# Kernel tuning notes

Hardware: AMD Instinct MI355X
Metric: run time of the kernel (lower is better)

## Reference

```python
import jax, jax.numpy as jnp
import numpy as np
import math

B, S, D, H, KVH = 4, 2048, 4096, 32, 8
HD = D // H          # 128
N_REP = H // KVH     # 4
MAX_S = 2048


def setup_inputs() -> dict:
    key = jax.random.key(0)
    ks = jax.random.split(key, 6)
    x = jax.random.normal(ks[0], (B, S, D), dtype=jnp.float32)
    sc = 0.02
    wq = jax.random.normal(ks[1], (D, H * HD), dtype=jnp.float32) * sc
    wk = jax.random.normal(ks[2], (D, KVH * HD), dtype=jnp.float32) * sc
    wv = jax.random.normal(ks[3], (D, KVH * HD), dtype=jnp.float32) * sc
    wo = jax.random.normal(ks[4], (H * HD, D), dtype=jnp.float32) * sc
    # RoPE tables (matches llama precompute_freqs_cis, theta=10000)
    inv_freq = 1.0 / (10000.0 ** (np.arange(0, HD, 2, dtype=np.float32) / HD))  # [HD/2]
    t = np.arange(S, dtype=np.float32)
    freqs = np.outer(t, inv_freq)  # [S, HD/2]
    cos = jnp.asarray(np.cos(freqs), dtype=jnp.float32)
    sin = jnp.asarray(np.sin(freqs), dtype=jnp.float32)
    cache_k = jnp.zeros((B, MAX_S, KVH, HD), dtype=jnp.float32)
    cache_v = jnp.zeros((B, MAX_S, KVH, HD), dtype=jnp.float32)
    return {"x": x, "wq": wq, "wk": wk, "wv": wv, "wo": wo,
            "cos": cos, "sin": sin, "cache_k": cache_k, "cache_v": cache_v,
            "start_pos": 0}


def _apply_rope(x, cos, sin):
    # x: [B, S, h, HD]; interleaved complex rotation, as torch view_as_complex
    xr = x.reshape(*x.shape[:-1], HD // 2, 2)
    x0, x1 = xr[..., 0], xr[..., 1]
    c = cos[None, :, None, :]
    s = sin[None, :, None, :]
    o0 = x0 * c - x1 * s
    o1 = x0 * s + x1 * c
    return jnp.stack([o0, o1], axis=-1).reshape(x.shape)


def reference(x, wq, wk, wv, wo, cos, sin, cache_k, cache_v, start_pos):
    bsz, seqlen, _ = x.shape
    xq = (x @ wq).reshape(bsz, seqlen, H, HD)
    xk = (x @ wk).reshape(bsz, seqlen, KVH, HD)
    xv = (x @ wv).reshape(bsz, seqlen, KVH, HD)
    xq = _apply_rope(xq, cos, sin)
    xk = _apply_rope(xk, cos, sin)
    # KV cache update then slice [:start_pos+seqlen]
    cache_k = jax.lax.dynamic_update_slice(cache_k, xk, (0, start_pos, 0, 0))
    cache_v = jax.lax.dynamic_update_slice(cache_v, xv, (0, start_pos, 0, 0))
    kv_len = start_pos + seqlen
    keys = cache_k[:, :kv_len]    # [B, K, KVH, HD]
    values = cache_v[:, :kv_len]
    # repeat_kv: expand kv heads by n_rep (GQA)
    keys = jnp.repeat(keys, N_REP, axis=2)      # [B, K, H, HD]
    values = jnp.repeat(values, N_REP, axis=2)
    scores = jnp.einsum('bqhd,bkhd->bhqk', xq, keys) / math.sqrt(HD)
    probs = jax.nn.softmax(scores.astype(jnp.float32), axis=-1).astype(xq.dtype)
    out = jnp.einsum('bhqk,bkhd->bqhd', probs, values)
    out = out.reshape(bsz, seqlen, H * HD)
    return out @ wo
```

## Files before the change

kernel.cpp:

```cpp
#include <hip/hip_runtime.h>
#include <math.h>
#include <stdint.h>

typedef unsigned short u16;
typedef __attribute__((ext_vector_type(8))) short short8;
typedef __attribute__((ext_vector_type(4))) float f32x4;

#define B_   4
#define S_   2048
#define D_   4096
#define H_   32
#define KVH_ 8
#define HD_  128
#define NQKV 6144
#define MTOT 8192
#define ATT_SCALE 0.08838834764831845f
#define DEFER_THR 90.5f

__device__ __forceinline__ float bf2f(u16 u) {
  unsigned x = ((unsigned)u) << 16;
  return __builtin_bit_cast(float, x);
}
__device__ __forceinline__ u16 f2bf(float f) {
  unsigned x = __builtin_bit_cast(unsigned, f);
  x += 0x7fffu + ((x >> 16) & 1u);
  return (u16)(x >> 16);
}
__device__ __forceinline__ unsigned pack2bf(float a, float b) {
  return (unsigned)f2bf(a) | ((unsigned)f2bf(b) << 16);
}

typedef const __attribute__((address_space(1))) void* gas1p;
typedef __attribute__((address_space(3))) void* las3p;
__device__ __forceinline__ void gload16(const void* g, void* l) {
  __builtin_amdgcn_global_load_lds((gas1p)g, (las3p)l, 16, 0, 0);
}

__device__ __forceinline__ int swz64(int row, int kc) {
  return row * 64 + ((kc ^ (row & 7)) << 3);
}
__device__ __forceinline__ int swz128(int row, int kc) {
  return row * 128 + ((kc ^ (row & 7)) << 3);
}

__global__ void cast_f32_to_bf16(const float* __restrict__ in, u16* __restrict__ out, long n) {
  long i = ((long)blockIdx.x * 256 + threadIdx.x) * 4;
  if (i >= n) return;
  float4 v = *(const float4*)(in + i);
  ushort4 o;
  o.x = f2bf(v.x); o.y = f2bf(v.y); o.z = f2bf(v.z); o.w = f2bf(v.w);
  *(ushort4*)(out + i) = o;
}

__global__ void transpose_cast(const float* __restrict__ in, u16* __restrict__ out, int K, int N) {
  __shared__ u16 tile[32][33];
  int n0 = blockIdx.x * 32, k0 = blockIdx.y * 32;
  int tx = threadIdx.x, ty = threadIdx.y;
  for (int i = ty; i < 32; i += 8)
    tile[i][tx] = f2bf(in[(long)(k0 + i) * N + n0 + tx]);
  __syncthreads();
  for (int i = ty; i < 32; i += 8)
    out[(long)(n0 + i) * K + k0 + tx] = tile[tx][i];
}

template <int OUTF32>
__global__ __launch_bounds__(512, 2) void gemm256(const u16* __restrict__ A,
                                                  const u16* __restrict__ BT,
                                                  void* __restrict__ Cout,
                                                  int M, int N, int K) {
  __shared__ u16 Ls[2][2][2][128 * 64];
  int tid = threadIdx.x, lane = tid & 63, wid = tid >> 6;
  int wm = wid >> 2, wn = wid & 3;
  int m0 = blockIdx.y * 256, n0 = blockIdx.x * 256;
  int frow = lane & 15, fk = lane >> 4;

  f32x4 acc[8][4];
#pragma unroll
  for (int i = 0; i < 8; i++)
#pragma unroll
    for (int j = 0; j < 4; j++) acc[i][j] = (f32x4){0.f, 0.f, 0.f, 0.f};

  int srow = lane >> 3;
  int sc = ((lane & 7) ^ srow) * 8;
  const u16* a0 = A + (long)(m0 + (2 * wid + 0) * 8 + srow) * K + sc;
  const u16* a1 = A + (long)(m0 + (2 * wid + 1) * 8 + srow) * K + sc;
  const u16* b0 = BT + (long)(n0 + (2 * wid + 0) * 8 + srow) * K + sc;
  const u16* b1 = BT + (long)(n0 + (2 * wid + 1) * 8 + srow) * K + sc;
  long hstep = (long)128 * K;

#define STAGE_A(buf, half, t) do {                                              \
    gload16(a0 + (half) * hstep + (long)(t) * 64, &Ls[buf][0][half][(2 * wid + 0) * 512]); \
    gload16(a1 + (half) * hstep + (long)(t) * 64, &Ls[buf][0][half][(2 * wid + 1) * 512]); \
  } while (0)
#define STAGE_B(buf, half, t) do {                                              \
    gload16(b0 + (half) * hstep + (long)(t) * 64, &Ls[buf][1][half][(2 * wid + 0) * 512]); \
    gload16(b1 + (half) * hstep + (long)(t) * 64, &Ls[buf][1][half][(2 * wid + 1) * 512]); \
  } while (0)

  int nk = K / 64;
  STAGE_A(0, 0, 0); STAGE_A(0, 1, 0); STAGE_B(0, 0, 0); STAGE_B(0, 1, 0);
  STAGE_B(1, 0, 1); STAGE_B(1, 1, 1);
  asm volatile("s_waitcnt vmcnt(4)" ::: "memory");
  __builtin_amdgcn_s_barrier();

#define PHASE(P, STAGE_STMT, VM_STMT)                                           \
  {                                                                             \
    short8 af[2][2];                                                            \
    _Pragma("unroll") for (int mm = 0; mm < 2; mm++)                            \
      _Pragma("unroll") for (int kk = 0; kk < 2; kk++)                          \
        af[mm][kk] = *(const short8*)&Ah[swz64((2 * (P) + mm) * 16 + frow, kk * 4 + fk)]; \
    STAGE_STMT;                                                                 \
    VM_STMT;                                                                    \
    __builtin_amdgcn_s_barrier();                                               \
    asm volatile("s_waitcnt lgkmcnt(0)" ::: "memory");                          \
    __builtin_amdgcn_sched_barrier(0);                                          \
    __builtin_amdgcn_s_setprio(1);                                              \
    _Pragma("unroll") for (int mm = 0; mm < 2; mm++)                            \
      _Pragma("unroll") for (int n = 0; n < 4; n++)                             \
        _Pragma("unroll") for (int kk = 0; kk < 2; kk++)                        \
          acc[2 * (P) + mm][n] = __builtin_amdgcn_mfma_f32_16x16x32_bf16(       \
              af[mm][kk], bfr[n][kk], acc[2 * (P) + mm][n], 0, 0, 0);           \
    __builtin_amdgcn_s_setprio(0);                                              \
    __builtin_amdgcn_s_barrier();                                               \
  }

  for (int t = 0; t < nk; ++t) {
    int pi = t & 1;
    const u16* Ah = &Ls[pi][0][wm][0];
    const u16* Bh = &Ls[pi][1][wn >> 1][0];
    int brow = (wn & 1) * 64;
    short8 bfr[4][2];
#pragma unroll
    for (int n = 0; n < 4; n++)
#pragma unroll
      for (int kk = 0; kk < 2; kk++)
        bfr[n][kk] = *(const short8*)&Bh[swz64(brow + n * 16 + frow, kk * 4 + fk)];

    PHASE(0, if (t + 1 < nk) STAGE_A(pi ^ 1, 0, t + 1), );
    PHASE(1, if (t + 1 < nk) STAGE_A(pi ^ 1, 1, t + 1), );
    PHASE(2, if (t + 2 < nk) STAGE_B(pi, 0, t + 2), );
    PHASE(3, if (t + 2 < nk) STAGE_B(pi, 1, t + 2),
          if (t + 2 < nk) { asm volatile("s_waitcnt vmcnt(4)" ::: "memory"); }
          else            { asm volatile("s_waitcnt vmcnt(0)" ::: "memory"); });
  }
#undef PHASE
#undef STAGE_A
#undef STAGE_B

  int cc = lane & 15, cr = fk * 4;
#pragma unroll
  for (int i = 0; i < 8; i++)
#pragma unroll
    for (int j = 0; j < 4; j++)
#pragma unroll
      for (int r = 0; r < 4; r++) {
        int m = m0 + wm * 128 + i * 16 + cr + r;
        int n = n0 + wn * 64 + j * 16 + cc;
        if (OUTF32)
          ((float*)Cout)[(long)m * N + n] = acc[i][j][r];
        else
          ((u16*)Cout)[(long)m * N + n] = f2bf(acc[i][j][r]);
      }
}

__global__ void rope_kernel(u16* __restrict__ qkv, const float* __restrict__ cosb,
                            const float* __restrict__ sinb, const int* __restrict__ start_pos) {
  long tid = (long)blockIdx.x * 256 + threadIdx.x;
  const long total = (long)MTOT * 2560;
  if (tid >= total) return;
  int row = (int)(tid / 2560);
  int p = (int)(tid % 2560);
  int col = (p < 2048) ? (p * 2) : (D_ + (p - 2048) * 2);
  int i = (col >> 1) & 63;
  int s = row & (S_ - 1);
  int pos = s + *start_pos;
  float c = cosb[pos * 64 + i];
  float sn = sinb[pos * 64 + i];
  u16* ptr = qkv + (long)row * NQKV + col;
  unsigned v = *(unsigned*)ptr;
  float x0 = bf2f((u16)(v & 0xffff));
  float x1 = bf2f((u16)(v >> 16));
  float o0 = x0 * c - x1 * sn;
  float o1 = x0 * sn + x1 * c;
  unsigned ov = (unsigned)f2bf(o0) | ((unsigned)f2bf(o1) << 16);
  *(unsigned*)ptr = ov;
}

__global__ void build_vt(const u16* __restrict__ qkv, u16* __restrict__ vt) {
  int bk = blockIdx.z;
  int b = bk >> 3, kvh = bk & 7;
  int s0 = blockIdx.x * 32, d0 = blockIdx.y * 32;
  __shared__ u16 tile[32][33];
  int tx = threadIdx.x, ty = threadIdx.y;
  const u16* src = qkv + (long)(b * S_) * NQKV + D_ + KVH_ * HD_ + kvh * HD_;
  for (int i = ty; i < 32; i += 8)
    tile[i][tx] = src[(long)(s0 + i) * NQKV + d0 + tx];
  __syncthreads();
  u16* dst = vt + ((long)(b * KVH_ + kvh) * HD_) * S_;
  for (int i = ty; i < 32; i += 8)
    dst[(long)(d0 + i) * S_ + s0 + tx] = tile[tx][i];
}

__global__ __launch_bounds__(256, 2) void attn_kernel(const u16* __restrict__ qkv,
                                                      const u16* __restrict__ vt,
                                                      u16* __restrict__ obuf) {
  int nb = gridDim.x;
  int fid = (int)((blockIdx.x & 7) * (nb >> 3) + (blockIdx.x >> 3));
  int bx = fid & 15;
  int bh = fid >> 4;
  int b = bh >> 5, h = bh & 31;
  int kvh = h >> 2;
  int q0 = bx * 128;
  int tid = threadIdx.x, lane = tid & 63, wid = tid >> 6;

  __shared__ u16 Ks[2][64 * 128];
  __shared__ u16 VTs[2][128 * 64];
  __shared__ u16 Ps[4][32 * 64];

  int frow = lane & 15;
  int fk = lane >> 4;

  short8 qf[2][4];
#pragma unroll
  for (int qq = 0; qq < 2; ++qq) {
    const u16* qbase = qkv + (long)(b * S_ + q0 + wid * 32 + qq * 16 + frow) * NQKV + h * HD_;
#pragma unroll
    for (int kd = 0; kd < 4; ++kd) qf[qq][kd] = *(const short8*)(qbase + kd * 32 + fk * 8);
  }

  f32x4 acc_o[2][8];
#pragma unroll
  for (int qq = 0; qq < 2; qq++)
#pragma unroll
    for (int i = 0; i < 8; i++) acc_o[qq][i] = (f32x4){0.f, 0.f, 0.f, 0.f};
  float m_r[2] = {-1e30f, -1e30f};
  float l_r[2] = {0.f, 0.f};

  const u16* kgl[4];
  const u16* vgl[4];
#pragma unroll
  for (int j = 0; j < 4; j++) {
    int gk = j * 4 + wid;
    int rk = gk * 4 + (lane >> 4);
    int ck = (lane & 15) ^ (rk & 7);
    kgl[j] = qkv + (long)(b * S_ + rk) * NQKV + D_ + kvh * HD_ + ck * 8;
    int gv = j * 4 + wid;
    int rv = gv * 8 + (lane >> 3);
    int cv = (lane & 7) ^ (rv & 7);
    vgl[j] = vt + ((long)(b * KVH_ + kvh) * HD_ + rv) * S_ + cv * 8;
  }

#define STAGE_KV(buf, t) do {                                                   \
    _Pragma("unroll") for (int j = 0; j < 4; j++) {                             \
      int g = j * 4 + wid;                                                      \
      gload16(kgl[j] + (long)((t) * 64) * NQKV, &Ks[buf][g * 512]);             \
      gload16(vgl[j] + (t) * 64, &VTs[buf][g * 512]);                           \
    }                                                                           \
  } while (0)

  const int ntiles = S_ / 64;
  STAGE_KV(0, 0);

  for (int t = 0; t < ntiles; ++t) {
    if (t + 1 < ntiles) {
      STAGE_KV((t + 1) & 1, t + 1);
      asm volatile("s_waitcnt vmcnt(8)" ::: "memory");
    } else {
      asm volatile("s_waitcnt vmcnt(0)" ::: "memory");
    }
    __builtin_amdgcn_s_barrier();
    __builtin_amdgcn_sched_barrier(0);
    const u16* Kb = &Ks[t & 1][0];
    const u16* Vb = &VTs[t & 1][0];

    f32x4 sc[4][2];
#pragma unroll
    for (int f = 0; f < 4; f++)
#pragma unroll
      for (int qq = 0; qq < 2; qq++) sc[f][qq] = (f32x4){0.f, 0.f, 0.f, 0.f};
#pragma unroll
    for (int f = 0; f < 4; f++)
#pragma unroll
      for (int kd = 0; kd < 4; kd++) {
        short8 kf = *(const short8*)&Kb[swz128(f * 16 + frow, kd * 4 + fk)];
        sc[f][0] = __builtin_amdgcn_mfma_f32_16x16x32_bf16(kf, qf[0][kd], sc[f][0], 0, 0, 0);
        sc[f][1] = __builtin_amdgcn_mfma_f32_16x16x32_bf16(kf, qf[1][kd], sc[f][1], 0, 0, 0);
      }

    float mx[2];
#pragma unroll
    for (int qq = 0; qq < 2; ++qq) {
      float m = sc[0][qq][0];
#pragma unroll
      for (int f = 0; f < 4; f++)
#pragma unroll
        for (int r = 0; r < 4; r++) m = fmaxf(m, sc[f][qq][r]);
      m = fmaxf(m, __shfl_xor(m, 16, 64));
      m = fmaxf(m, __shfl_xor(m, 32, 64));
      mx[qq] = m;
    }
    if (!__all((mx[0] <= m_r[0] + DEFER_THR) && (mx[1] <= m_r[1] + DEFER_THR))) {
#pragma unroll
      for (int qq = 0; qq < 2; ++qq) {
        float mnew = fmaxf(m_r[qq], mx[qq]);
        float scl = __expf((m_r[qq] - mnew) * ATT_SCALE);
        l_r[qq] *= scl;
        m_r[qq] = mnew;
#pragma unroll
        for (int df = 0; df < 8; df++) acc_o[qq][df] *= scl;
      }
    }

#pragma unroll
    for (int qq = 0; qq < 2; ++qq) {
      float nms = -m_r[qq] * ATT_SCALE;
      float rs = 0.f;
      int prow = qq * 16 + frow;
      int pbase = prow * 64 + (fk & 1) * 4;
      int q7 = frow & 7;
#pragma unroll
      for (int f = 0; f < 4; f++) {
        float p0 = __expf(fmaf(sc[f][qq][0], ATT_SCALE, nms));
        float p1 = __expf(fmaf(sc[f][qq][1], ATT_SCALE, nms));
        float p2 = __expf(fmaf(sc[f][qq][2], ATT_SCALE, nms));
        float p3 = __expf(fmaf(sc[f][qq][3], ATT_SCALE, nms));
        rs += (p0 + p1) + (p2 + p3);
        unsigned lo = pack2bf(p0, p1);
        unsigned hi = pack2bf(p2, p3);
        int chunk = (f * 2 + (fk >> 1)) ^ q7;
        uint2 wv2; wv2.x = lo; wv2.y = hi;
        *(uint2*)&Ps[wid][pbase + (chunk << 3)] = wv2;
      }
      rs += __shfl_xor(rs, 16, 64);
      rs += __shfl_xor(rs, 32, 64);
      l_r[qq] += rs;
    }

    asm volatile("s_waitcnt lgkmcnt(0)" ::: "memory");
    __builtin_amdgcn_sched_barrier(0);

    short8 pf[2][2];
#pragma unroll
    for (int qq = 0; qq < 2; qq++)
#pragma unroll
      for (int kk = 0; kk < 2; kk++)
        pf[qq][kk] = *(const short8*)&Ps[wid][(qq * 16 + frow) * 64 + (((kk * 4 + fk) ^ (frow & 7)) << 3)];
#pragma unroll
    for (int df = 0; df < 8; df++)
#pragma unroll
      for (int kk = 0; kk < 2; kk++) {
        short8 vf = *(const short8*)&Vb[swz64(df * 16 + frow, kk * 4 + fk)];
        acc_o[0][df] = __builtin_amdgcn_mfma_f32_16x16x32_bf16(vf, pf[0][kk], acc_o[0][df], 0, 0, 0);
        acc_o[1][df] = __builtin_amdgcn_mfma_f32_16x16x32_bf16(vf, pf[1][kk], acc_o[1][df], 0, 0, 0);
      }
    __syncthreads();
  }
#undef STAGE_KV

#pragma unroll
  for (int qq = 0; qq < 2; ++qq) {
    float inv = 1.0f / l_r[qq];
    long srow = (long)(b * S_ + q0 + wid * 32 + qq * 16 + frow);
    u16* orow = obuf + srow * D_ + h * HD_ + fk * 4;
#pragma unroll
    for (int df = 0; df < 8; df++) {
      uint2 ov;
      ov.x = pack2bf(acc_o[qq][df][0] * inv, acc_o[qq][df][1] * inv);
      ov.y = pack2bf(acc_o[qq][df][2] * inv, acc_o[qq][df][3] * inv);
      *(uint2*)(orow + df * 16) = ov;
    }
  }
}

extern "C" void kernel_launch(void* const* d_in, const int* in_sizes, int n_in,
                              void* d_out, int out_size, void* d_ws, size_t ws_size,
                              hipStream_t stream) {
  const float* x = (const float*)d_in[0];
  const float* wq = (const float*)d_in[1];
  const float* wk = (const float*)d_in[2];
  const float* wv = (const float*)d_in[3];
  const float* wo = (const float*)d_in[4];
  const float* cosb = (const float*)d_in[5];
  const float* sinb = (const float*)d_in[6];
  const int* start_pos = (const int*)d_in[9];
  float* out = (float*)d_out;

  char* ws = (char*)d_ws;
  u16* xb = (u16*)ws;
  u16* wqkvT = (u16*)(ws + 67108864L);
  u16* woT = (u16*)(ws + 117440512L);
  u16* qkvb = (u16*)(ws + 150994944L);
  u16* vtb = (u16*)(ws + 251658240L);
  u16* obuf = xb;

  cast_f32_to_bf16<<<dim3(32768), dim3(256), 0, stream>>>(x, xb, (long)MTOT * D_);

  transpose_cast<<<dim3(128, 128), dim3(32, 8), 0, stream>>>(wq, wqkvT, D_, 4096);
  transpose_cast<<<dim3(32, 128), dim3(32, 8), 0, stream>>>(wk, wqkvT + (long)4096 * D_, D_, 1024);
  transpose_cast<<<dim3(32, 128), dim3(32, 8), 0, stream>>>(wv, wqkvT + (long)5120 * D_, D_, 1024);
  transpose_cast<<<dim3(128, 128), dim3(32, 8), 0, stream>>>(wo, woT, D_, 4096);

  gemm256<0><<<dim3(NQKV / 256, MTOT / 256), dim3(512), 0, stream>>>(xb, wqkvT, qkvb, MTOT, NQKV, D_);

  rope_kernel<<<dim3(81920), dim3(256), 0, stream>>>(qkvb, cosb, sinb, start_pos);

  build_vt<<<dim3(64, 4, 32), dim3(32, 8), 0, stream>>>(qkvb, vtb);

  attn_kernel<<<dim3(2048), dim3(256), 0, stream>>>(qkvb, vtb, obuf);

  gemm256<1><<<dim3(D_ / 256, MTOT / 256), dim3(512), 0, stream>>>(obuf, woT, out, MTOT, D_, D_);
}
```

Before: 1.051 ms.

## Fuse Q RoPE into attention Q load, use exp2 and hardware bf16 packing

Query RoPE now runs inside the attention kernel as Q fragments are loaded into registers, so the standalone RoPE pass only rotates the K columns and moves about a fifth of the data it did before. Softmax exponentials switch from __expf to exp2f with the log2(e) factor folded into the scale. Float-to-bf16 packing uses the HIP bf16x2 intrinsic instead of manual rounding, and the row-max reduction becomes a tree. The attention prologue gains extra cos/sin loads per Q row, which is small next to the K/V loop.

```diff
diff --git a/kernel.cpp b/kernel.cpp
--- a/kernel.cpp
+++ b/kernel.cpp
@@ -1,4 +1,5 @@
 #include <hip/hip_runtime.h>
+#include <hip/hip_bf16.h>
 #include <math.h>
 #include <stdint.h>
 
@@ -15,6 +16,7 @@
 #define NQKV 6144
 #define MTOT 8192
 #define ATT_SCALE 0.08838834764831845f
+#define SCL2 (ATT_SCALE * 1.4426950408889634f)
 #define DEFER_THR 90.5f
 
 __device__ __forceinline__ float bf2f(u16 u) {
@@ -26,8 +28,11 @@
   x += 0x7fffu + ((x >> 16) & 1u);
   return (u16)(x >> 16);
 }
-__device__ __forceinline__ unsigned pack2bf(float a, float b) {
-  return (unsigned)f2bf(a) | ((unsigned)f2bf(b) << 16);
+__device__ __forceinline__ unsigned pk2(float a, float b) {
+  __hip_bfloat162 h = __float22bfloat162_rn(float2{a, b});
+  unsigned r;
+  __builtin_memcpy(&r, &h, 4);
+  return r;
 }
 
 typedef const __attribute__((address_space(1))) void* gas1p;
@@ -163,15 +168,15 @@
       }
 }
 
-__global__ void rope_kernel(u16* __restrict__ qkv, const float* __restrict__ cosb,
-                            const float* __restrict__ sinb, const int* __restrict__ start_pos) {
+__global__ void rope_k_kernel(u16* __restrict__ qkv, const float* __restrict__ cosb,
+                              const float* __restrict__ sinb, const int* __restrict__ start_pos) {
   long tid = (long)blockIdx.x * 256 + threadIdx.x;
-  const long total = (long)MTOT * 2560;
+  const long total = (long)MTOT * 512;
   if (tid >= total) return;
-  int row = (int)(tid / 2560);
-  int p = (int)(tid % 2560);
-  int col = (p < 2048) ? (p * 2) : (D_ + (p - 2048) * 2);
-  int i = (col >> 1) & 63;
+  int row = (int)(tid >> 9);
+  int p = (int)(tid & 511);
+  int col = D_ + p * 2;
+  int i = p & 63;
   int s = row & (S_ - 1);
   int pos = s + *start_pos;
   float c = cosb[pos * 64 + i];
@@ -182,8 +187,7 @@
   float x1 = bf2f((u16)(v >> 16));
   float o0 = x0 * c - x1 * sn;
   float o1 = x0 * sn + x1 * c;
-  unsigned ov = (unsigned)f2bf(o0) | ((unsigned)f2bf(o1) << 16);
-  *(unsigned*)ptr = ov;
+  *(unsigned*)ptr = pk2(o0, o1);
 }
 
 __global__ void build_vt(const u16* __restrict__ qkv, u16* __restrict__ vt) {
@@ -203,7 +207,10 @@
 
 __global__ __launch_bounds__(256, 2) void attn_kernel(const u16* __restrict__ qkv,
                                                       const u16* __restrict__ vt,
-                                                      u16* __restrict__ obuf) {
+                                                      u16* __restrict__ obuf,
+                                                      const float* __restrict__ cosb,
+                                                      const float* __restrict__ sinb,
+                                                      const int* __restrict__ start_pos) {
   int nb = gridDim.x;
   int fid = (int)((blockIdx.x & 7) * (nb >> 3) + (blockIdx.x >> 3));
   int bx = fid & 15;
@@ -223,9 +230,24 @@
   short8 qf[2][4];
 #pragma unroll
   for (int qq = 0; qq < 2; ++qq) {
-    const u16* qbase = qkv + (long)(b * S_ + q0 + wid * 32 + qq * 16 + frow) * NQKV + h * HD_;
-#pragma unroll
-    for (int kd = 0; kd < 4; ++kd) qf[qq][kd] = *(const short8*)(qbase + kd * 32 + fk * 8);
+    int s = q0 + wid * 32 + qq * 16 + frow;
+    int pos = s + *start_pos;
+    const float* cb = cosb + pos * 64;
+    const float* sb = sinb + pos * 64;
+    const u16* qbase = qkv + (long)(b * S_ + s) * NQKV + h * HD_;
+#pragma unroll
+    for (int kd = 0; kd < 4; ++kd) {
+      short8 v = *(const short8*)(qbase + kd * 32 + fk * 8);
+      union { short8 s8; unsigned u[4]; } w;
+#pragma unroll
+      for (int j = 0; j < 4; ++j) {
+        int i = kd * 16 + fk * 4 + j;
+        float c = cb[i], sn = sb[i];
+        float x0 = bf2f((u16)v[2 * j]), x1 = bf2f((u16)v[2 * j + 1]);
+        w.u[j] = pk2(x0 * c - x1 * sn, x0 * sn + x1 * c);
+      }
+      qf[qq][kd] = w.s8;
+    }
   }
 
   f32x4 acc_o[2][8];
@@ -290,11 +312,11 @@
     float mx[2];
 #pragma unroll
     for (int qq = 0; qq < 2; ++qq) {
-      float m = sc[0][qq][0];
+      float mf[4];
 #pragma unroll
       for (int f = 0; f < 4; f++)
-#pragma unroll
-        for (int r = 0; r < 4; r++) m = fmaxf(m, sc[f][qq][r]);
+        mf[f] = fmaxf(fmaxf(sc[f][qq][0], sc[f][qq][1]), fmaxf(sc[f][qq][2], sc[f][qq][3]));
+      float m = fmaxf(fmaxf(mf[0], mf[1]), fmaxf(mf[2], mf[3]));
       m = fmaxf(m, __shfl_xor(m, 16, 64));
       m = fmaxf(m, __shfl_xor(m, 32, 64));
       mx[qq] = m;
@@ -303,7 +325,7 @@
 #pragma unroll
       for (int qq = 0; qq < 2; ++qq) {
         float mnew = fmaxf(m_r[qq], mx[qq]);
-        float scl = __expf((m_r[qq] - mnew) * ATT_SCALE);
+        float scl = exp2f((m_r[qq] - mnew) * SCL2);
         l_r[qq] *= scl;
         m_r[qq] = mnew;
 #pragma unroll
@@ -313,22 +335,20 @@
 
 #pragma unroll
     for (int qq = 0; qq < 2; ++qq) {
-      float nms = -m_r[qq] * ATT_SCALE;
+      float nms = -m_r[qq] * SCL2;
       float rs = 0.f;
       int prow = qq * 16 + frow;
       int pbase = prow * 64 + (fk & 1) * 4;
       int q7 = frow & 7;
 #pragma unroll
       for (int f = 0; f < 4; f++) {
-        float p0 = __expf(fmaf(sc[f][qq][0], ATT_SCALE, nms));
-        float p1 = __expf(fmaf(sc[f][qq][1], ATT_SCALE, nms));
-        float p2 = __expf(fmaf(sc[f][qq][2], ATT_SCALE, nms));
-        float p3 = __expf(fmaf(sc[f][qq][3], ATT_SCALE, nms));
+        float p0 = exp2f(fmaf(sc[f][qq][0], SCL2, nms));
+        float p1 = exp2f(fmaf(sc[f][qq][1], SCL2, nms));
+        float p2 = exp2f(fmaf(sc[f][qq][2], SCL2, nms));
+        float p3 = exp2f(fmaf(sc[f][qq][3], SCL2, nms));
         rs += (p0 + p1) + (p2 + p3);
-        unsigned lo = pack2bf(p0, p1);
-        unsigned hi = pack2bf(p2, p3);
         int chunk = (f * 2 + (fk >> 1)) ^ q7;
-        uint2 wv2; wv2.x = lo; wv2.y = hi;
+        uint2 wv2; wv2.x = pk2(p0, p1); wv2.y = pk2(p2, p3);
         *(uint2*)&Ps[wid][pbase + (chunk << 3)] = wv2;
       }
       rs += __shfl_xor(rs, 16, 64);
@@ -365,8 +385,8 @@
 #pragma unroll
     for (int df = 0; df < 8; df++) {
       uint2 ov;
-      ov.x = pack2bf(acc_o[qq][df][0] * inv, acc_o[qq][df][1] * inv);
-      ov.y = pack2bf(acc_o[qq][df][2] * inv, acc_o[qq][df][3] * inv);
+      ov.x = pk2(acc_o[qq][df][0] * inv, acc_o[qq][df][1] * inv);
+      ov.y = pk2(acc_o[qq][df][2] * inv, acc_o[qq][df][3] * inv);
       *(uint2*)(orow + df * 16) = ov;
     }
   }
@@ -402,11 +422,11 @@
 
   gemm256<0><<<dim3(NQKV / 256, MTOT / 256), dim3(512), 0, stream>>>(xb, wqkvT, qkvb, MTOT, NQKV, D_);
 
-  rope_kernel<<<dim3(81920), dim3(256), 0, stream>>>(qkvb, cosb, sinb, start_pos);
+  rope_k_kernel<<<dim3(16384), dim3(256), 0, stream>>>(qkvb, cosb, sinb, start_pos);
 
   build_vt<<<dim3(64, 4, 32), dim3(32, 8), 0, stream>>>(qkvb, vtb);
 
-  attn_kernel<<<dim3(2048), dim3(256), 0, stream>>>(qkvb, vtb, obuf);
+  attn_kernel<<<dim3(2048), dim3(256), 0, stream>>>(qkvb, vtb, obuf, cosb, sinb, start_pos);
 
   gemm256<1><<<dim3(D_ / 256, MTOT / 256), dim3(512), 0, stream>>>(obuf, woT, out, MTOT, D_, D_);
 }
```

Result: no change. 1.062 ms (+1.1%).
